# Kernel optimization log

Measured on AMD Instinct MI355X. Metric: run time of the kernel, lower is better.

The kernel has to match this reference:

```python
import jax, jax.numpy as jnp
import numpy as np

N_NODES = 100000
N_EDGES = 3200000
IN_CH, HID, OUT_CH = 128, 16, 64


def gcn_conv(x, W, b, row, col, n_nodes):
    # PyG GCNConv: add self loops, symmetric deg^{-1/2} normalization,
    # linear transform, scatter-add aggregation at target nodes (col).
    x = x @ W  # [N, out]
    deg = jax.ops.segment_sum(jnp.ones_like(col, dtype=x.dtype), col,
                              num_segments=n_nodes)  # includes self loops
    inv_sqrt = jnp.where(deg > 0, jax.lax.rsqrt(deg), 0.0)
    norm = inv_sqrt[row] * inv_sqrt[col]  # [E+N]
    msgs = x[row] * norm[:, None]  # gather + scale
    out = jax.ops.segment_sum(msgs, col, num_segments=n_nodes)
    return out + b


def setup_inputs() -> dict:
    key = jax.random.key(0)
    ks = jax.random.split(key, 12)
    x = jax.random.normal(ks[0], (N_NODES, IN_CH), dtype=jnp.float32)
    edge_index = jax.random.randint(ks[1], (2, N_EDGES), 0, N_NODES, dtype=jnp.int64)

    def glorot(k, fan_in, fan_out):
        s = jnp.sqrt(6.0 / (fan_in + fan_out))
        return jax.random.uniform(k, (fan_in, fan_out), jnp.float32, -s, s)

    return {
        'x': x,
        'edge_index': edge_index,
        'conv1_W': glorot(ks[2], IN_CH, HID),
        'conv1_b': jnp.zeros((HID,), jnp.float32),
        'conv2_W': glorot(ks[3], HID, OUT_CH),
        'conv2_b': jnp.zeros((OUT_CH,), jnp.float32),
        't1_W': glorot(ks[4], IN_CH, HID),
        't1_b': jnp.zeros((HID,), jnp.float32),
        't2_W': glorot(ks[5], HID, OUT_CH),
        't2_b': jnp.zeros((OUT_CH,), jnp.float32),
    }


def reference(x, edge_index, conv1_W, conv1_b, conv2_W, conv2_b,
              t1_W, t1_b, t2_W, t2_b):
    n = x.shape[0]
    # add self loops once (fixed shape)
    loops = jnp.arange(n, dtype=edge_index.dtype)
    row = jnp.concatenate([edge_index[0], loops])
    col = jnp.concatenate([edge_index[1], loops])

    identity1 = x @ t1_W + t1_b
    h = jax.nn.relu(gcn_conv(x, conv1_W, conv1_b, row, col, n)) + identity1
    identity2 = h @ t2_W + t2_b
    out = jax.nn.relu(gcn_conv(h, conv2_W, conv2_b, row, col, n)) + identity2
    return out
```

## Files before the change

kernel.cpp:

```cpp
#include <hip/hip_runtime.h>

#define INCH 128
#define C1   16
#define C2   64
#define LOCB 7
#define BNODES (1 << LOCB)
#define CAP  8192
#define ROWBITS 17
#define ROWMASK ((1 << ROWBITS) - 1)
#define SENT 0xFFFFFFFFu
#define BSLACK 384

typedef int iv4 __attribute__((ext_vector_type(4)));
typedef unsigned short usv8 __attribute__((ext_vector_type(8)));

__device__ __forceinline__ unsigned short f2bf(float f) {
    unsigned u = __float_as_uint(f);
    return (unsigned short)((u + 0x7FFF + ((u >> 16) & 1)) >> 16);
}
__device__ __forceinline__ float bf2f(unsigned short s) {
    return __uint_as_float((unsigned)s << 16);
}

__global__ void binit_kernel(int* __restrict__ gcur, int K,
                             int* __restrict__ xz, int* __restrict__ hz) {
    int t = blockIdx.x * blockDim.x + threadIdx.x;
    if (t < K) gcur[t] = t * CAP;
    if (blockIdx.x == 0 && threadIdx.x < 8) {
        xz[threadIdx.x] = 0;
        hz[threadIdx.x] = 0;
    }
}

__global__ __launch_bounds__(256) void bucket_kernel(
    const int* __restrict__ row, const int* __restrict__ col,
    int* __restrict__ gcur, int* __restrict__ barr,
    int e, int n, int K, int nblocks)
{
    __shared__ int cnt[1024];
    __shared__ int cur[1024];
    __shared__ int sst[1024];
    int e4 = e >> 2;
    long b0 = (long)blockIdx.x * e4 / nblocks;
    long b1 = (long)(blockIdx.x + 1) * e4 / nblocks;
    const iv4* c4p = (const iv4*)col;
    const iv4* r4p = (const iv4*)row;
    for (int i = threadIdx.x; i < 1024; i += 256) cnt[i] = 0;
    __syncthreads();
    for (long i = b0 + threadIdx.x; i < b1; i += 256) {
        iv4 c4 = c4p[i], r4 = r4p[i];
        #pragma unroll
        for (int k = 0; k < 4; ++k) {
            unsigned c = (unsigned)c4[k], r = (unsigned)r4[k];
            if (c < (unsigned)n && r < (unsigned)n)
                atomicAdd(&cnt[c >> LOCB], 1);
        }
    }
    if (blockIdx.x == 0) {
        for (int i = e4 * 4 + threadIdx.x; i < e; i += 256) {
            unsigned c = (unsigned)col[i], r = (unsigned)row[i];
            if (c < (unsigned)n && r < (unsigned)n)
                atomicAdd(&cnt[c >> LOCB], 1);
        }
    }
    __syncthreads();
    for (int i = threadIdx.x; i < K; i += 256) {
        int c = cnt[i];
        int start = c ? atomicAdd(&gcur[i], (c + 15) & ~15) : 0;
        cur[i] = start;
        sst[i] = start;
    }
    __syncthreads();
    for (long i = b0 + threadIdx.x; i < b1; i += 256) {
        iv4 c4 = c4p[i], r4 = r4p[i];
        #pragma unroll
        for (int k = 0; k < 4; ++k) {
            unsigned c = (unsigned)c4[k], r = (unsigned)r4[k];
            if (c < (unsigned)n && r < (unsigned)n) {
                int b = c >> LOCB;
                int slot = atomicAdd(&cur[b], 1);
                if ((unsigned)slot < (unsigned)((b + 1) * CAP))
                    barr[slot] = (int)(r | ((c & (BNODES - 1)) << ROWBITS));
            }
        }
    }
    if (blockIdx.x == 0) {
        for (int i = e4 * 4 + threadIdx.x; i < e; i += 256) {
            unsigned c = (unsigned)col[i], r = (unsigned)row[i];
            if (c < (unsigned)n && r < (unsigned)n) {
                int b = c >> LOCB;
                int slot = atomicAdd(&cur[b], 1);
                if ((unsigned)slot < (unsigned)((b + 1) * CAP))
                    barr[slot] = (int)(r | ((c & (BNODES - 1)) << ROWBITS));
            }
        }
    }
    __syncthreads();
    for (int i = threadIdx.x; i < K; i += 256) {
        int c = cnt[i];
        if (!c) continue;
        int start = sst[i];
        int end = start + c;
        int re  = start + ((c + 15) & ~15);
        int lim = (i + 1) * CAP;
        if (end > lim) end = lim;
        if (re  > lim) re  = lim;
        for (int j = end; j < re; ++j) barr[j] = (int)SENT;
    }
}

__global__ __launch_bounds__(1024) void bucket_scan_kernel(
    const int* __restrict__ gcur, int* __restrict__ bbase, int K)
{
    __shared__ int tmp[1024];
    int t = threadIdx.x;
    int len = 0;
    if (t < K) {
        int l = gcur[t] - t * CAP;
        len = (l < 0) ? 0 : (l > CAP ? CAP : l);
        len += BSLACK;
    }
    tmp[t] = len;
    __syncthreads();
    for (int off = 1; off < 1024; off <<= 1) {
        int v = (t >= off) ? tmp[t - off] : 0;
        __syncthreads();
        tmp[t] += v;
        __syncthreads();
    }
    if (t < K) bbase[t] = tmp[t] - len;
}

__global__ __launch_bounds__(256) void sort_kernel(
    const int* __restrict__ barr, const int* __restrict__ gcur,
    const int* __restrict__ bbase,
    int* __restrict__ cnt, int* __restrict__ offs, float* __restrict__ inv,
    int* __restrict__ sorted, int n)
{
    __shared__ int lcnt[BNODES];
    __shared__ int lcur[BNODES];
    __shared__ int tmp[BNODES];
    int b = blockIdx.x;
    int tid = threadIdx.x;
    if (tid < BNODES) lcnt[tid] = 0;
    __syncthreads();
    int base = b * CAP;
    int len = gcur[b] - base;
    if (len < 0) len = 0;
    if (len > CAP) len = CAP;
    int len4 = len >> 2;
    const iv4* b4 = (const iv4*)(barr + base);
    for (int i = tid; i < len4; i += 256) {
        iv4 p4 = b4[i];
        #pragma unroll
        for (int k = 0; k < 4; ++k) {
            unsigned pk = (unsigned)p4[k];
            if ((pk & ROWMASK) < (unsigned)n)
                atomicAdd(&lcnt[(pk >> ROWBITS) & (BNODES - 1)], 1);
        }
    }
    for (int i = len4 * 4 + tid; i < len; i += 256) {
        unsigned pk = (unsigned)barr[base + i];
        if ((pk & ROWMASK) < (unsigned)n)
            atomicAdd(&lcnt[(pk >> ROWBITS) & (BNODES - 1)], 1);
    }
    __syncthreads();
    int v  = (tid < BNODES) ? lcnt[tid] : 0;
    int pc = (v + 3) & ~3;
    if (tid < BNODES) tmp[tid] = pc;
    __syncthreads();
    for (int off = 1; off < BNODES; off <<= 1) {
        int t2 = (tid < BNODES && tid >= off) ? tmp[tid - off] : 0;
        __syncthreads();
        if (tid < BNODES) tmp[tid] += t2;
        __syncthreads();
    }
    int gbase = bbase[b];
    if (tid < BNODES) {
        int exc = tmp[tid] - pc;
        lcur[tid] = exc;
        int node = (b << LOCB) + tid;
        if (node < n) {
            cnt[node]  = v;
            offs[node] = gbase + exc;
            inv[node]  = rsqrtf((float)(v + 1));
        }
        for (int j = v; j < pc; ++j)
            sorted[gbase + exc + j] = n;
    }
    __syncthreads();
    for (int i = tid; i < len4; i += 256) {
        iv4 p4 = b4[i];
        #pragma unroll
        for (int k = 0; k < 4; ++k) {
            unsigned pk = (unsigned)p4[k];
            if ((pk & ROWMASK) < (unsigned)n) {
                int loc = (pk >> ROWBITS) & (BNODES - 1);
                int pos = atomicAdd(&lcur[loc], 1);
                if ((unsigned)pos < (unsigned)(CAP + BSLACK))
                    sorted[gbase + pos] = (int)(pk & ROWMASK);
            }
        }
    }
    for (int i = len4 * 4 + tid; i < len; i += 256) {
        unsigned pk = (unsigned)barr[base + i];
        if ((pk & ROWMASK) < (unsigned)n) {
            int loc = (pk >> ROWBITS) & (BNODES - 1);
            int pos = atomicAdd(&lcur[loc], 1);
            if ((unsigned)pos < (unsigned)(CAP + BSLACK))
                sorted[gbase + pos] = (int)(pk & ROWMASK);
        }
    }
}

__global__ __launch_bounds__(256) void linear1_kernel(
    const float* __restrict__ x, const float* __restrict__ W1,
    const float* __restrict__ T1, const float* __restrict__ t1b,
    const float* __restrict__ inv,
    unsigned short* __restrict__ xW1s_bf, float* __restrict__ xT1, int n)
{
    __shared__ float Wc[INCH][32];
    __shared__ float xs[16][INCH + 4];
    int tid = threadIdx.x;

    for (int i = tid; i < INCH * C1; i += 256) {
        int k = i / C1, c = i % C1;
        Wc[k][c]      = W1[i];
        Wc[k][c + 16] = T1[i];
    }
    int node0 = blockIdx.x * 16;
    for (int i = tid; i < 16 * (INCH / 4); i += 256) {
        int r = i / (INCH / 4);
        int cc = i % (INCH / 4);
        int node = node0 + r;
        float4 v = make_float4(0.f, 0.f, 0.f, 0.f);
        if (node < n) v = ((const float4*)x)[(size_t)node * (INCH / 4) + cc];
        ((float4*)&xs[r][0])[cc] = v;
    }
    __syncthreads();

    int ch = tid & 15, nl = tid >> 4;
    int node = node0 + nl;
    if (node >= n) return;
    float a1 = 0.f, a2 = 0.f;
    #pragma unroll
    for (int k = 0; k < INCH; ++k) {
        float xv = xs[nl][k];
        a1 += xv * Wc[k][ch];
        a2 += xv * Wc[k][ch + 16];
    }
    xW1s_bf[(node << 4) + ch] = f2bf(a1 * inv[node]);
    xT1[(node << 4) + ch]     = a2 + t1b[ch];
}

#define GATHER_ACC(SRCBUF)                                                    \
    float a0 = 0.f, a1 = 0.f, a2 = 0.f, a3 = 0.f,                             \
          a4 = 0.f, a5 = 0.f, a6 = 0.f, a7 = 0.f;                             \
    {                                                                         \
        int p  = beg + (pr << 2);                                             \
        int pe = beg + m;                                                     \
        for (; p + 3 < pe; p += 8) {                                          \
            iv4 s4 = *(const iv4*)(sorted + p);              \
            usv8 v0 = *(const usv8*)(SRCBUF + ((size_t)(unsigned)s4[0] << 4) + chb); \
            usv8 v1 = *(const usv8*)(SRCBUF + ((size_t)(unsigned)s4[1] << 4) + chb); \
            usv8 v2 = *(const usv8*)(SRCBUF + ((size_t)(unsigned)s4[2] << 4) + chb); \
            usv8 v3 = *(const usv8*)(SRCBUF + ((size_t)(unsigned)s4[3] << 4) + chb); \
            a0 += bf2f(v0[0]) + bf2f(v1[0]) + bf2f(v2[0]) + bf2f(v3[0]);      \
            a1 += bf2f(v0[1]) + bf2f(v1[1]) + bf2f(v2[1]) + bf2f(v3[1]);      \
            a2 += bf2f(v0[2]) + bf2f(v1[2]) + bf2f(v2[2]) + bf2f(v3[2]);      \
            a3 += bf2f(v0[3]) + bf2f(v1[3]) + bf2f(v2[3]) + bf2f(v3[3]);      \
            a4 += bf2f(v0[4]) + bf2f(v1[4]) + bf2f(v2[4]) + bf2f(v3[4]);      \
            a5 += bf2f(v0[5]) + bf2f(v1[5]) + bf2f(v2[5]) + bf2f(v3[5]);      \
            a6 += bf2f(v0[6]) + bf2f(v1[6]) + bf2f(v2[6]) + bf2f(v3[6]);      \
            a7 += bf2f(v0[7]) + bf2f(v1[7]) + bf2f(v2[7]) + bf2f(v3[7]);      \
        }                                                                     \
    }                                                                         \
    a0 += __shfl_xor(a0, 2); a1 += __shfl_xor(a1, 2);                         \
    a2 += __shfl_xor(a2, 2); a3 += __shfl_xor(a3, 2);                         \
    a4 += __shfl_xor(a4, 2); a5 += __shfl_xor(a5, 2);                         \
    a6 += __shfl_xor(a6, 2); a7 += __shfl_xor(a7, 2);

__global__ __launch_bounds__(256) void agg1_csr_kernel(
    const int* __restrict__ sorted, const int* __restrict__ offs,
    const int* __restrict__ cnt, const float* __restrict__ inv,
    const unsigned short* __restrict__ xW1s_bf, const float* __restrict__ xT1,
    const float* __restrict__ b1,
    float* __restrict__ h, unsigned short* __restrict__ hs_bf, int n)
{
    int tid = threadIdx.x;
    int node = blockIdx.x * 64 + (tid >> 2);
    int pr  = (tid >> 1) & 1;
    int chb = (tid & 1) << 3;
    int beg = 0, m = 0;
    if (node < n) { beg = offs[node]; m = (cnt[node] + 3) & ~3; }

    GATHER_ACC(xW1s_bf)

    if (node >= n || pr != 0) return;
    size_t idx = ((size_t)node << 4) + chb;
    usv8 selfv = *(const usv8*)(xW1s_bf + idx);
    float ic = inv[node];
    float hv0 = fmaxf((a0 + bf2f(selfv[0])) * ic + b1[chb + 0], 0.f) + xT1[idx + 0];
    float hv1 = fmaxf((a1 + bf2f(selfv[1])) * ic + b1[chb + 1], 0.f) + xT1[idx + 1];
    float hv2 = fmaxf((a2 + bf2f(selfv[2])) * ic + b1[chb + 2], 0.f) + xT1[idx + 2];
    float hv3 = fmaxf((a3 + bf2f(selfv[3])) * ic + b1[chb + 3], 0.f) + xT1[idx + 3];
    float hv4 = fmaxf((a4 + bf2f(selfv[4])) * ic + b1[chb + 4], 0.f) + xT1[idx + 4];
    float hv5 = fmaxf((a5 + bf2f(selfv[5])) * ic + b1[chb + 5], 0.f) + xT1[idx + 5];
    float hv6 = fmaxf((a6 + bf2f(selfv[6])) * ic + b1[chb + 6], 0.f) + xT1[idx + 6];
    float hv7 = fmaxf((a7 + bf2f(selfv[7])) * ic + b1[chb + 7], 0.f) + xT1[idx + 7];
    ((float4*)(h + idx))[0] = make_float4(hv0, hv1, hv2, hv3);
    ((float4*)(h + idx))[1] = make_float4(hv4, hv5, hv6, hv7);
    usv8 hb;
    hb[0] = f2bf(hv0 * ic); hb[1] = f2bf(hv1 * ic);
    hb[2] = f2bf(hv2 * ic); hb[3] = f2bf(hv3 * ic);
    hb[4] = f2bf(hv4 * ic); hb[5] = f2bf(hv5 * ic);
    hb[6] = f2bf(hv6 * ic); hb[7] = f2bf(hv7 * ic);
    *(usv8*)(hs_bf + idx) = hb;
}

__global__ __launch_bounds__(256) void agg2_fused_kernel(
    const int* __restrict__ sorted, const int* __restrict__ offs,
    const int* __restrict__ cnt, const float* __restrict__ inv,
    const unsigned short* __restrict__ hs_bf, const float* __restrict__ h,
    const float* __restrict__ W2, const float* __restrict__ T2,
    const float* __restrict__ b2, const float* __restrict__ t2b,
    float* __restrict__ out, int n)
{
    __shared__ float Wc[C1][128];
    __shared__ float acc_s[64][C1];
    __shared__ float h_s[64][C1];
    int tid = threadIdx.x;

    for (int i = tid; i < C1 * 128; i += 256) {
        int k = i >> 7, c = i & 127;
        Wc[k][c] = (c < 64) ? W2[k * C2 + c] : T2[k * C2 + (c - 64)];
    }
    {
        int node0 = blockIdx.x * 64;
        if (tid < 256) {
            float4 v = make_float4(0.f, 0.f, 0.f, 0.f);
            if (node0 + (tid >> 2) < n)
                v = ((const float4*)h)[(size_t)node0 * 4 + tid];
            ((float4*)&h_s[0][0])[tid] = v;
        }
    }

    int node = blockIdx.x * 64 + (tid >> 2);
    int pr  = (tid >> 1) & 1;
    int chb = (tid & 1) << 3;
    int beg = 0, m = 0;
    if (node < n) { beg = offs[node]; m = (cnt[node] + 3) & ~3; }

    GATHER_ACC(hs_bf)

    if (node < n && pr == 0) {
        size_t idx = ((size_t)node << 4) + chb;
        usv8 selfv = *(const usv8*)(hs_bf + idx);
        float ic = inv[node];
        int loc = tid >> 2;
        float4* ap = (float4*)&acc_s[loc][chb];
        ap[0] = make_float4((a0 + bf2f(selfv[0])) * ic, (a1 + bf2f(selfv[1])) * ic,
                            (a2 + bf2f(selfv[2])) * ic, (a3 + bf2f(selfv[3])) * ic);
        ap[1] = make_float4((a4 + bf2f(selfv[4])) * ic, (a5 + bf2f(selfv[5])) * ic,
                            (a6 + bf2f(selfv[6])) * ic, (a7 + bf2f(selfv[7])) * ic);
    }
    __syncthreads();

    int och = tid & 63, g = tid >> 6;
    float w1r[C1], w2r[C1];
    #pragma unroll
    for (int k = 0; k < C1; ++k) { w1r[k] = Wc[k][och]; w2r[k] = Wc[k][och + 64]; }
    float bb = b2[och], tb = t2b[och];
    for (int q = 0; q < 16; ++q) {
        int loc = (g << 4) + q;
        int node2 = blockIdx.x * 64 + loc;
        if (node2 >= n) continue;
        float s1 = bb, s2 = tb;
        #pragma unroll
        for (int k = 0; k < C1; ++k) {
            s1 += acc_s[loc][k] * w1r[k];
            s2 += h_s[loc][k]   * w2r[k];
        }
        out[(size_t)node2 * C2 + och] = fmaxf(s1, 0.f) + s2;
    }
}

extern "C" void kernel_launch(void* const* d_in, const int* in_sizes, int n_in,
                              void* d_out, int out_size, void* d_ws, size_t ws_size,
                              hipStream_t stream) {
    const float* x   = (const float*)d_in[0];
    const int*   ei  = (const int*)d_in[1];
    const float* W1  = (const float*)d_in[2];
    const float* b1  = (const float*)d_in[3];
    const float* W2  = (const float*)d_in[4];
    const float* b2  = (const float*)d_in[5];
    const float* T1  = (const float*)d_in[6];
    const float* t1b = (const float*)d_in[7];
    const float* T2  = (const float*)d_in[8];
    const float* t2b = (const float*)d_in[9];
    float* out = (float*)d_out;

    const int n = in_sizes[0] / INCH;
    const int e = in_sizes[1] / 2;
    const int* row = ei;
    const int* col = ei + e;
    const int K = (n + BNODES - 1) >> LOCB;

    char* ws = (char*)d_ws;
    int*   gcur  = (int*)ws;                          ws += 4096;
    int*   bbase = (int*)ws;                          ws += 4096;
    int*   cnt   = (int*)ws;                          ws += (size_t)n * 4;
    int*   offs  = (int*)ws;                          ws += (size_t)n * 4;
    float* inv   = (float*)ws;                        ws += (size_t)n * 4;
    float* xT1   = (float*)ws;                        ws += (size_t)n * C1 * 4;
    float* h     = (float*)ws;                        ws += (size_t)n * C1 * 4;
    unsigned short* xW1s_bf = (unsigned short*)ws;    ws += (size_t)n * C1 * 2 + 64;
    unsigned short* hs_bf   = (unsigned short*)ws;    ws += (size_t)n * C1 * 2 + 64;
    int*   sorted= (int*)ws;                          ws += ((size_t)K * CAP + (size_t)K * BSLACK) * 4;
    int*   barr  = (int*)ws;                          ws += (size_t)K * CAP * 4;

    const int B = 256;
    const int nbb = 390;

    binit_kernel      <<<(K + B - 1) / B, B, 0, stream>>>(gcur, K,
                        (int*)(xW1s_bf + (size_t)n * C1), (int*)(hs_bf + (size_t)n * C1));
    bucket_kernel     <<<nbb, B, 0, stream>>>(row, col, gcur, barr, e, n, K, nbb);
    bucket_scan_kernel<<<1, 1024, 0, stream>>>(gcur, bbase, K);
    sort_kernel       <<<K, B, 0, stream>>>(barr, gcur, bbase, cnt, offs, inv, sorted, n);

    linear1_kernel <<<(n + 15) / 16, B, 0, stream>>>(x, W1, T1, t1b, inv, xW1s_bf, xT1, n);
    agg1_csr_kernel<<<(n + 63) / 64, B, 0, stream>>>(sorted, offs, cnt, inv, xW1s_bf, xT1, b1, h, hs_bf, n);

    agg2_fused_kernel<<<(n + 63) / 64, B, 0, stream>>>(sorted, offs, cnt, inv, hs_bf, h,
                                                       W2, T2, b2, t2b, out, n);
}
```

Baseline: 272.9 us.

## Replace two-level bucket sort CSR build with global-atomic counting sort

```diff
diff --git a/kernel.cpp b/kernel.cpp
--- a/kernel.cpp
+++ b/kernel.cpp
@@ -3,13 +3,6 @@
 #define INCH 128
 #define C1   16
 #define C2   64
-#define LOCB 7
-#define BNODES (1 << LOCB)
-#define CAP  8192
-#define ROWBITS 17
-#define ROWMASK ((1 << ROWBITS) - 1)
-#define SENT 0xFFFFFFFFu
-#define BSLACK 384
 
 typedef int iv4 __attribute__((ext_vector_type(4)));
 typedef unsigned short usv8 __attribute__((ext_vector_type(8)));
@@ -22,65 +15,99 @@
     return __uint_as_float((unsigned)s << 16);
 }
 
-__global__ void binit_kernel(int* __restrict__ gcur, int K,
-                             int* __restrict__ xz, int* __restrict__ hz) {
+__global__ __launch_bounds__(256) void init_kernel(
+    int* __restrict__ deg, int n, int* __restrict__ xz, int* __restrict__ hz)
+{
     int t = blockIdx.x * blockDim.x + threadIdx.x;
-    if (t < K) gcur[t] = t * CAP;
-    if (blockIdx.x == 0 && threadIdx.x < 8) {
-        xz[threadIdx.x] = 0;
-        hz[threadIdx.x] = 0;
-    }
-}
-
-__global__ __launch_bounds__(256) void bucket_kernel(
+    if (t < n) deg[t] = 0;
+    if (t < 8) { xz[t] = 0; hz[t] = 0; }
+}
+
+__global__ __launch_bounds__(256) void deg_kernel(
     const int* __restrict__ row, const int* __restrict__ col,
-    int* __restrict__ gcur, int* __restrict__ barr,
-    int e, int n, int K, int nblocks)
-{
-    __shared__ int cnt[1024];
-    __shared__ int cur[1024];
-    __shared__ int sst[1024];
+    int* __restrict__ deg, int e, int n)
+{
     int e4 = e >> 2;
-    long b0 = (long)blockIdx.x * e4 / nblocks;
-    long b1 = (long)(blockIdx.x + 1) * e4 / nblocks;
     const iv4* c4p = (const iv4*)col;
     const iv4* r4p = (const iv4*)row;
-    for (int i = threadIdx.x; i < 1024; i += 256) cnt[i] = 0;
-    __syncthreads();
-    for (long i = b0 + threadIdx.x; i < b1; i += 256) {
+    int stride = gridDim.x * blockDim.x;
+    for (int i = blockIdx.x * blockDim.x + threadIdx.x; i < e4; i += stride) {
         iv4 c4 = c4p[i], r4 = r4p[i];
         #pragma unroll
         for (int k = 0; k < 4; ++k) {
             unsigned c = (unsigned)c4[k], r = (unsigned)r4[k];
             if (c < (unsigned)n && r < (unsigned)n)
-                atomicAdd(&cnt[c >> LOCB], 1);
+                atomicAdd(&deg[c], 1);
         }
     }
     if (blockIdx.x == 0) {
         for (int i = e4 * 4 + threadIdx.x; i < e; i += 256) {
             unsigned c = (unsigned)col[i], r = (unsigned)row[i];
             if (c < (unsigned)n && r < (unsigned)n)
-                atomicAdd(&cnt[c >> LOCB], 1);
-        }
-    }
+                atomicAdd(&deg[c], 1);
+        }
+    }
+}
+
+__global__ __launch_bounds__(1024) void scan1_kernel(
+    const int* __restrict__ deg, int* __restrict__ offs,
+    int* __restrict__ btot, int n)
+{
+    __shared__ int tmp[1024];
+    int tid = threadIdx.x;
+    int node = blockIdx.x * 1024 + tid;
+    int d  = (node < n) ? deg[node] : 0;
+    int pc = (d + 3) & ~3;
+    tmp[tid] = pc;
     __syncthreads();
-    for (int i = threadIdx.x; i < K; i += 256) {
-        int c = cnt[i];
-        int start = c ? atomicAdd(&gcur[i], (c + 15) & ~15) : 0;
-        cur[i] = start;
-        sst[i] = start;
-    }
-    __syncthreads();
-    for (long i = b0 + threadIdx.x; i < b1; i += 256) {
+    for (int off = 1; off < 1024; off <<= 1) {
+        int v = (tid >= off) ? tmp[tid - off] : 0;
+        __syncthreads();
+        tmp[tid] += v;
+        __syncthreads();
+    }
+    if (node < n) offs[node] = tmp[tid] - pc;
+    if (tid == 1023) btot[blockIdx.x] = tmp[1023];
+}
+
+__global__ void scan2_kernel(int* __restrict__ btot, int nb) {
+    if (blockIdx.x == 0 && threadIdx.x == 0) {
+        int s = 0;
+        for (int i = 0; i < nb; ++i) { int v = btot[i]; btot[i] = s; s += v; }
+    }
+}
+
+__global__ __launch_bounds__(1024) void scan3_kernel(
+    const int* __restrict__ deg, int* __restrict__ offs, int* __restrict__ cur,
+    float* __restrict__ inv, int* __restrict__ sorted,
+    const int* __restrict__ btot, int n)
+{
+    int node = blockIdx.x * 1024 + threadIdx.x;
+    if (node >= n) return;
+    int o = offs[node] + btot[blockIdx.x];
+    offs[node] = o;
+    cur[node]  = o;
+    int d = deg[node], pc = (d + 3) & ~3;
+    for (int j = d; j < pc; ++j) sorted[o + j] = n;
+    inv[node] = rsqrtf((float)(d + 1));
+}
+
+__global__ __launch_bounds__(256) void scatter_kernel(
+    const int* __restrict__ row, const int* __restrict__ col,
+    int* __restrict__ cur, int* __restrict__ sorted, int e, int n, int cap)
+{
+    int e4 = e >> 2;
+    const iv4* c4p = (const iv4*)col;
+    const iv4* r4p = (const iv4*)row;
+    int stride = gridDim.x * blockDim.x;
+    for (int i = blockIdx.x * blockDim.x + threadIdx.x; i < e4; i += stride) {
         iv4 c4 = c4p[i], r4 = r4p[i];
         #pragma unroll
         for (int k = 0; k < 4; ++k) {
             unsigned c = (unsigned)c4[k], r = (unsigned)r4[k];
             if (c < (unsigned)n && r < (unsigned)n) {
-                int b = c >> LOCB;
-                int slot = atomicAdd(&cur[b], 1);
-                if ((unsigned)slot < (unsigned)((b + 1) * CAP))
-                    barr[slot] = (int)(r | ((c & (BNODES - 1)) << ROWBITS));
+                int pos = atomicAdd(&cur[c], 1);
+                if ((unsigned)pos < (unsigned)cap) sorted[pos] = (int)r;
             }
         }
     }
@@ -88,127 +115,9 @@
         for (int i = e4 * 4 + threadIdx.x; i < e; i += 256) {
             unsigned c = (unsigned)col[i], r = (unsigned)row[i];
             if (c < (unsigned)n && r < (unsigned)n) {
-                int b = c >> LOCB;
-                int slot = atomicAdd(&cur[b], 1);
-                if ((unsigned)slot < (unsigned)((b + 1) * CAP))
-                    barr[slot] = (int)(r | ((c & (BNODES - 1)) << ROWBITS));
+                int pos = atomicAdd(&cur[c], 1);
+                if ((unsigned)pos < (unsigned)cap) sorted[pos] = (int)r;
             }
-        }
-    }
-    __syncthreads();
-    for (int i = threadIdx.x; i < K; i += 256) {
-        int c = cnt[i];
-        if (!c) continue;
-        int start = sst[i];
-        int end = start + c;
-        int re  = start + ((c + 15) & ~15);
-        int lim = (i + 1) * CAP;
-        if (end > lim) end = lim;
-        if (re  > lim) re  = lim;
-        for (int j = end; j < re; ++j) barr[j] = (int)SENT;
-    }
-}
-
-__global__ __launch_bounds__(1024) void bucket_scan_kernel(
-    const int* __restrict__ gcur, int* __restrict__ bbase, int K)
-{
-    __shared__ int tmp[1024];
-    int t = threadIdx.x;
-    int len = 0;
-    if (t < K) {
-        int l = gcur[t] - t * CAP;
-        len = (l < 0) ? 0 : (l > CAP ? CAP : l);
-        len += BSLACK;
-    }
-    tmp[t] = len;
-    __syncthreads();
-    for (int off = 1; off < 1024; off <<= 1) {
-        int v = (t >= off) ? tmp[t - off] : 0;
-        __syncthreads();
-        tmp[t] += v;
-        __syncthreads();
-    }
-    if (t < K) bbase[t] = tmp[t] - len;
-}
-
-__global__ __launch_bounds__(256) void sort_kernel(
-    const int* __restrict__ barr, const int* __restrict__ gcur,
-    const int* __restrict__ bbase,
-    int* __restrict__ cnt, int* __restrict__ offs, float* __restrict__ inv,
-    int* __restrict__ sorted, int n)
-{
-    __shared__ int lcnt[BNODES];
-    __shared__ int lcur[BNODES];
-    __shared__ int tmp[BNODES];
-    int b = blockIdx.x;
-    int tid = threadIdx.x;
-    if (tid < BNODES) lcnt[tid] = 0;
-    __syncthreads();
-    int base = b * CAP;
-    int len = gcur[b] - base;
-    if (len < 0) len = 0;
-    if (len > CAP) len = CAP;
-    int len4 = len >> 2;
-    const iv4* b4 = (const iv4*)(barr + base);
-    for (int i = tid; i < len4; i += 256) {
-        iv4 p4 = b4[i];
-        #pragma unroll
-        for (int k = 0; k < 4; ++k) {
-            unsigned pk = (unsigned)p4[k];
-            if ((pk & ROWMASK) < (unsigned)n)
-                atomicAdd(&lcnt[(pk >> ROWBITS) & (BNODES - 1)], 1);
-        }
-    }
-    for (int i = len4 * 4 + tid; i < len; i += 256) {
-        unsigned pk = (unsigned)barr[base + i];
-        if ((pk & ROWMASK) < (unsigned)n)
-            atomicAdd(&lcnt[(pk >> ROWBITS) & (BNODES - 1)], 1);
-    }
-    __syncthreads();
-    int v  = (tid < BNODES) ? lcnt[tid] : 0;
-    int pc = (v + 3) & ~3;
-    if (tid < BNODES) tmp[tid] = pc;
-    __syncthreads();
-    for (int off = 1; off < BNODES; off <<= 1) {
-        int t2 = (tid < BNODES && tid >= off) ? tmp[tid - off] : 0;
-        __syncthreads();
-        if (tid < BNODES) tmp[tid] += t2;
-        __syncthreads();
-    }
-    int gbase = bbase[b];
-    if (tid < BNODES) {
-        int exc = tmp[tid] - pc;
-        lcur[tid] = exc;
-        int node = (b << LOCB) + tid;
-        if (node < n) {
-            cnt[node]  = v;
-            offs[node] = gbase + exc;
-            inv[node]  = rsqrtf((float)(v + 1));
-        }
-        for (int j = v; j < pc; ++j)
-            sorted[gbase + exc + j] = n;
-    }
-    __syncthreads();
-    for (int i = tid; i < len4; i += 256) {
-        iv4 p4 = b4[i];
-        #pragma unroll
-        for (int k = 0; k < 4; ++k) {
-            unsigned pk = (unsigned)p4[k];
-            if ((pk & ROWMASK) < (unsigned)n) {
-                int loc = (pk >> ROWBITS) & (BNODES - 1);
-                int pos = atomicAdd(&lcur[loc], 1);
-                if ((unsigned)pos < (unsigned)(CAP + BSLACK))
-                    sorted[gbase + pos] = (int)(pk & ROWMASK);
-            }
-        }
-    }
-    for (int i = len4 * 4 + tid; i < len; i += 256) {
-        unsigned pk = (unsigned)barr[base + i];
-        if ((pk & ROWMASK) < (unsigned)n) {
-            int loc = (pk >> ROWBITS) & (BNODES - 1);
-            int pos = atomicAdd(&lcur[loc], 1);
-            if ((unsigned)pos < (unsigned)(CAP + BSLACK))
-                sorted[gbase + pos] = (int)(pk & ROWMASK);
         }
     }
 }
@@ -404,33 +313,34 @@
     const int e = in_sizes[1] / 2;
     const int* row = ei;
     const int* col = ei + e;
-    const int K = (n + BNODES - 1) >> LOCB;
+    const int NB = (n + 1023) / 1024;
+    const int scap = e + 4 * n;
 
     char* ws = (char*)d_ws;
-    int*   gcur  = (int*)ws;                          ws += 4096;
-    int*   bbase = (int*)ws;                          ws += 4096;
-    int*   cnt   = (int*)ws;                          ws += (size_t)n * 4;
+    int*   deg   = (int*)ws;                          ws += (size_t)n * 4;
     int*   offs  = (int*)ws;                          ws += (size_t)n * 4;
+    int*   cur   = (int*)ws;                          ws += (size_t)n * 4;
     float* inv   = (float*)ws;                        ws += (size_t)n * 4;
+    int*   btot  = (int*)ws;                          ws += 4096;
     float* xT1   = (float*)ws;                        ws += (size_t)n * C1 * 4;
     float* h     = (float*)ws;                        ws += (size_t)n * C1 * 4;
     unsigned short* xW1s_bf = (unsigned short*)ws;    ws += (size_t)n * C1 * 2 + 64;
     unsigned short* hs_bf   = (unsigned short*)ws;    ws += (size_t)n * C1 * 2 + 64;
-    int*   sorted= (int*)ws;                          ws += ((size_t)K * CAP + (size_t)K * BSLACK) * 4;
-    int*   barr  = (int*)ws;                          ws += (size_t)K * CAP * 4;
+    int*   sorted= (int*)ws;                          ws += (size_t)scap * 4;
 
     const int B = 256;
-    const int nbb = 390;
-
-    binit_kernel      <<<(K + B - 1) / B, B, 0, stream>>>(gcur, K,
-                        (int*)(xW1s_bf + (size_t)n * C1), (int*)(hs_bf + (size_t)n * C1));
-    bucket_kernel     <<<nbb, B, 0, stream>>>(row, col, gcur, barr, e, n, K, nbb);
-    bucket_scan_kernel<<<1, 1024, 0, stream>>>(gcur, bbase, K);
-    sort_kernel       <<<K, B, 0, stream>>>(barr, gcur, bbase, cnt, offs, inv, sorted, n);
+
+    init_kernel   <<<(n + B - 1) / B, B, 0, stream>>>(deg, n,
+                    (int*)(xW1s_bf + (size_t)n * C1), (int*)(hs_bf + (size_t)n * C1));
+    deg_kernel    <<<768, B, 0, stream>>>(row, col, deg, e, n);
+    scan1_kernel  <<<NB, 1024, 0, stream>>>(deg, offs, btot, n);
+    scan2_kernel  <<<1, 64, 0, stream>>>(btot, NB);
+    scan3_kernel  <<<NB, 1024, 0, stream>>>(deg, offs, cur, inv, sorted, btot, n);
+    scatter_kernel<<<768, B, 0, stream>>>(row, col, cur, sorted, e, n, scap);
 
     linear1_kernel <<<(n + 15) / 16, B, 0, stream>>>(x, W1, T1, t1b, inv, xW1s_bf, xT1, n);
-    agg1_csr_kernel<<<(n + 63) / 64, B, 0, stream>>>(sorted, offs, cnt, inv, xW1s_bf, xT1, b1, h, hs_bf, n);
-
-    agg2_fused_kernel<<<(n + 63) / 64, B, 0, stream>>>(sorted, offs, cnt, inv, hs_bf, h,
+    agg1_csr_kernel<<<(n + 63) / 64, B, 0, stream>>>(sorted, offs, deg, inv, xW1s_bf, xT1, b1, h, hs_bf, n);
+
+    agg2_fused_kernel<<<(n + 63) / 64, B, 0, stream>>>(sorted, offs, deg, inv, hs_bf, h,
                                                        W2, T2, b2, t2b, out, n);
 }
```

After: 597.7 us. 2.19x slower.
